# Kernel tuning notes

Hardware: AMD Instinct MI355X
Metric: run time of the kernel (lower is better)

Reference implementation:

```python
import jax, jax.numpy as jnp
import numpy as np

NUM_CODEBOOKS = 8
CODEBOOK_SIZE = 2048
CODEBOOK_DIM = 16
HIDDEN_SIZE = 2048
CODEC_VOCAB_START = 0
PAD_IDX = 0


def setup_inputs() -> dict:
    key = jax.random.key(0)
    k_ids, k_emb, k_w1, k_b1, k_w2, k_b2 = jax.random.split(key, 6)
    B, S = 4, 4096
    codec_input_ids = jax.random.randint(
        k_ids, (B, S), 0, NUM_CODEBOOKS * CODEBOOK_SIZE, dtype=jnp.int64
    )
    # frozen embedding table; padding_idx row is zero
    embed_table = jax.random.normal(
        k_emb, (NUM_CODEBOOKS * CODEBOOK_SIZE, CODEBOOK_DIM), dtype=jnp.float32
    )
    embed_table = embed_table.at[PAD_IDX].set(0.0)
    # per-codebook projector params (stacked over codebook axis k)
    s1 = 1.0 / np.sqrt(CODEBOOK_DIM)
    s2 = 1.0 / np.sqrt(HIDDEN_SIZE)
    W1 = jax.random.uniform(k_w1, (NUM_CODEBOOKS, CODEBOOK_DIM, HIDDEN_SIZE), jnp.float32, -s1, s1)
    b1 = jax.random.uniform(k_b1, (NUM_CODEBOOKS, HIDDEN_SIZE), jnp.float32, -s1, s1)
    W2 = jax.random.uniform(k_w2, (NUM_CODEBOOKS, HIDDEN_SIZE, HIDDEN_SIZE), jnp.float32, -s2, s2)
    b2 = jax.random.uniform(k_b2, (NUM_CODEBOOKS, HIDDEN_SIZE), jnp.float32, -s2, s2)
    return {
        "codec_input_ids": codec_input_ids,
        "embed_table": embed_table,
        "W1": W1,
        "b1": b1,
        "W2": W2,
        "b2": b2,
    }


def reference(codec_input_ids, embed_table, W1, b1, W2, b2):
    ids = codec_input_ids - CODEC_VOCAB_START          # [B, S]
    embeds = embed_table[ids]                          # [B, S, D]
    cb = ids // CODEBOOK_SIZE                          # which codebook each token belongs to
    out = jnp.zeros(ids.shape + (HIDDEN_SIZE,), dtype=embeds.dtype)
    # fixed small loop over structurally distinct per-codebook projectors;
    # disjoint masks cover all tokens, so masked accumulation == torch scatter
    for k in range(NUM_CODEBOOKS):
        h = jnp.einsum("bsd,dh->bsh", embeds, W1[k]) + b1[k]
        h = jax.nn.gelu(h, approximate=False)          # torch nn.GELU default = exact
        h = jnp.einsum("bsh,hg->bsg", h, W2[k]) + b2[k]
        out = out + jnp.where((cb == k)[..., None], h, 0.0)
    return out
```

## Files before the change

### kernel.cpp

```cpp
#include <hip/hip_runtime.h>
#include <hip/hip_bf16.h>
#include <stdint.h>

#define NUM_CB   8
#define CB_BITS  11
#define DIM      16
#define HS       2048
#define NTOK     16384

#define BM 128
#define BN 128
#define BK 32
#define MAXT 160
#define PADCAP (136*BM)

#define OFF_CNT    0u
#define OFF_CUR    32u
#define OFF_NT     64u
#define OFF_GS     96u
#define OFF_TCB    128u
#define OFF_TROW   768u
#define OFF_TVAL   1408u
#define OFF_PERM   2048u
#define OFF_H      71680u
#define OFF_W2T    71374848u
#define WS_NEED    138483712u

typedef __attribute__((ext_vector_type(8))) short s16x8;
typedef __attribute__((ext_vector_type(4))) float f32x4;

__device__ __forceinline__ void load_lds16(const void* g, void* l) {
    __builtin_amdgcn_global_load_lds(
        (const __attribute__((address_space(1))) uint32_t*)g,
        (__attribute__((address_space(3))) uint32_t*)l, 16, 0, 0);
}

extern "C" __global__ void k_countplan(const int* __restrict__ ids,
                                       uint32_t* __restrict__ cur, uint32_t* __restrict__ numT,
                                       uint32_t* __restrict__ tcb, uint32_t* __restrict__ trow,
                                       uint32_t* __restrict__ tval, uint32_t* __restrict__ gstart) {
    __shared__ uint32_t hist[NUM_CB];
    __shared__ uint32_t s_tcb[MAXT], s_trow[MAXT], s_tval[MAXT];
    __shared__ uint32_t s_gs[NUM_CB], s_nt;
    const int tid = threadIdx.x;
    if (tid < NUM_CB) { hist[tid] = 0; cur[tid] = 0; }
    __syncthreads();
    for (int i = tid; i < NTOK; i += 1024)
        atomicAdd(&hist[(uint32_t)ids[i] >> CB_BITS], 1u);
    __syncthreads();
    if (tid == 0) {
        uint32_t ps = 0, nt = 0;
        for (int k = 0; k < NUM_CB; ++k) {
            s_gs[k] = ps;
            uint32_t c = hist[k];
            uint32_t tiles = (c + BM - 1) / BM;
            for (uint32_t m = 0; m < tiles; ++m) {
                s_tcb[nt] = (uint32_t)k;
                s_trow[nt] = ps + m * BM;
                uint32_t rem = c - m * BM;
                s_tval[nt] = rem < BM ? rem : BM;
                ++nt;
            }
            ps += tiles * BM;
        }
        s_nt = nt;
    }
    __syncthreads();
    const uint32_t nt = s_nt;
    if (tid < MAXT) {
        tcb[tid]  = (tid < (int)nt) ? s_tcb[tid] : 0u;
        trow[tid] = (tid < (int)nt) ? s_trow[tid] : 0u;
        tval[tid] = (tid < (int)nt) ? s_tval[tid] : 0u;
    }
    if (tid < NUM_CB) gstart[tid] = s_gs[tid];
    if (tid == 0) *numT = nt;
}

extern "C" __global__ void k_assign(const int* __restrict__ ids, const uint32_t* __restrict__ gstart,
                                    uint32_t* __restrict__ cur, uint32_t* __restrict__ perm) {
    __shared__ uint32_t lh[NUM_CB], lbase[NUM_CB];
    const int tid = threadIdx.x;
    const int t = blockIdx.x * 256 + tid;
    if (tid < NUM_CB) lh[tid] = 0;
    __syncthreads();
    const int cb = (uint32_t)ids[t] >> CB_BITS;
    atomicAdd(&lh[cb], 1u);
    __syncthreads();
    if (tid < NUM_CB) {
        lbase[tid] = lh[tid] ? atomicAdd(&cur[tid], lh[tid]) : 0u;
        lh[tid] = 0;
    }
    __syncthreads();
    const uint32_t r = atomicAdd(&lh[cb], 1u);
    perm[gstart[cb] + lbase[cb] + r] = (uint32_t)t;
}

extern "C" __global__ void k_hbuild(const int* __restrict__ ids, const float* __restrict__ emb,
                                    const float* __restrict__ W1, const float* __restrict__ b1,
                                    const uint32_t* __restrict__ numT, const uint32_t* __restrict__ tcb,
                                    const uint32_t* __restrict__ trow, const uint32_t* __restrict__ tval,
                                    const uint32_t* __restrict__ perm, __hip_bfloat16* __restrict__ H) {
    if (blockIdx.x >= *numT) return;
    const int cb = (int)tcb[blockIdx.x];
    const int row0 = (int)trow[blockIdx.x];
    const int valid = (int)tval[blockIdx.x];
    const int col0 = blockIdx.y * 256;
    const int tid = threadIdx.x;

    __shared__ float es[BM][DIM];
    __shared__ float w1s[DIM][256];
    __shared__ int   rid[BM];

    if (tid < BM) rid[tid] = (tid < valid) ? ids[perm[row0 + tid]] : 0;
    __syncthreads();
    for (int idx = tid; idx < BM * DIM; idx += 256) {
        int r = idx >> 4, d = idx & 15;
        es[r][d] = emb[(size_t)rid[r] * DIM + d];
    }
    const float* W1k = W1 + (size_t)cb * DIM * HS + col0;
    for (int idx = tid; idx < DIM * 256; idx += 256) {
        int d = idx >> 8, c = idx & 255;
        w1s[d][c] = W1k[(size_t)d * HS + c];
    }
    __syncthreads();

    float w[DIM];
    #pragma unroll
    for (int d = 0; d < DIM; ++d) w[d] = w1s[d][tid];
    const float bb = b1[(size_t)cb * HS + col0 + tid];
    __hip_bfloat16* Hc = H + (size_t)row0 * HS + col0 + tid;

    for (int r = 0; r < BM; ++r) {
        const float4 e0 = *(const float4*)&es[r][0];
        const float4 e1 = *(const float4*)&es[r][4];
        const float4 e2 = *(const float4*)&es[r][8];
        const float4 e3 = *(const float4*)&es[r][12];
        float acc = bb;
        acc += e0.x*w[0] + e0.y*w[1] + e0.z*w[2] + e0.w*w[3];
        acc += e1.x*w[4] + e1.y*w[5] + e1.z*w[6] + e1.w*w[7];
        acc += e2.x*w[8] + e2.y*w[9] + e2.z*w[10] + e2.w*w[11];
        acc += e3.x*w[12] + e3.y*w[13] + e3.z*w[14] + e3.w*w[15];
        float g = 0.5f * acc * (1.f + erff(acc * 0.70710678118f));
        Hc[(size_t)r * HS] = __float2bfloat16(g);
    }
}

extern "C" __global__ void k_w2t(const float* __restrict__ W2, __hip_bfloat16* __restrict__ W2T) {
    __shared__ float s[64][65];
    const int k0 = blockIdx.x * 64, n0 = blockIdx.y * 64, cb = blockIdx.z;
    const int tid = threadIdx.x;
    const float* src = W2 + ((size_t)cb << 22);
    #pragma unroll
    for (int i = 0; i < 16; ++i) {
        int idx = i * 256 + tid;
        int kl = idx >> 6, nl = idx & 63;
        s[kl][nl] = src[(size_t)(k0 + kl) * HS + n0 + nl];
    }
    __syncthreads();
    __hip_bfloat16* dst = W2T + ((size_t)cb << 22);
    #pragma unroll
    for (int i = 0; i < 16; ++i) {
        int idx = i * 256 + tid;
        int nl = idx >> 6, kl = idx & 63;
        dst[(size_t)(n0 + nl) * HS + k0 + kl] = __float2bfloat16(s[kl][nl]);
    }
}

extern "C" __global__ void __launch_bounds__(256, 4) k_gemm(
    const __hip_bfloat16* __restrict__ Hb, const __hip_bfloat16* __restrict__ W2Tb,
    const float* __restrict__ b2, const uint32_t* __restrict__ numT,
    const uint32_t* __restrict__ tcb, const uint32_t* __restrict__ trow,
    const uint32_t* __restrict__ tval, const uint32_t* __restrict__ perm,
    float* __restrict__ out)
{
    const int mslot = blockIdx.y;
    if (mslot >= (int)*numT) return;
    const int cb = (int)tcb[mslot];
    const int row0 = (int)trow[mslot];
    const int valid = (int)tval[mslot];
    const int n0 = blockIdx.x * BN;

    const int tid = threadIdx.x;
    const int lane = tid & 63, wave = tid >> 6;
    const int wm = wave >> 1, wn = wave & 1;

    __shared__ __align__(16) unsigned short As[2][4096];
    __shared__ __align__(16) unsigned short Bs[2][4096];

    const unsigned short* H = (const unsigned short*)Hb;
    const unsigned short* W2 = (const unsigned short*)W2Tb;

    const int idx0 = tid, idx1 = 256 + tid;
    const unsigned short* gA0 = H + (size_t)(row0 + (idx0 & 127)) * HS + (idx0 >> 7) * 8;
    const unsigned short* gA1 = H + (size_t)(row0 + (idx1 & 127)) * HS + (idx1 >> 7) * 8;
    const unsigned short* gB0 = W2 + ((size_t)cb * HS + n0 + (idx0 & 127)) * HS + (idx0 >> 7) * 8;
    const unsigned short* gB1 = W2 + ((size_t)cb * HS + n0 + (idx1 & 127)) * HS + (idx1 >> 7) * 8;

    const uint32_t ls0 = (uint32_t)__builtin_amdgcn_readfirstlane(wave * 512);
    const uint32_t ls1 = (uint32_t)__builtin_amdgcn_readfirstlane(2048 + wave * 512);

    f32x4 acc[4][4];
    #pragma unroll
    for (int i = 0; i < 4; ++i)
        #pragma unroll
        for (int j = 0; j < 4; ++j) acc[i][j] = (f32x4){0.f, 0.f, 0.f, 0.f};

    load_lds16(gA0, &As[0][ls0]);
    load_lds16(gA1, &As[0][ls1]);
    load_lds16(gB0, &Bs[0][ls0]);
    load_lds16(gB1, &Bs[0][ls1]);
    __syncthreads();

    const int c = lane >> 4, r = lane & 15;
    uint32_t aoff[4], boff[4];
    #pragma unroll
    for (int f = 0; f < 4; ++f) {
        aoff[f] = c * 1024 + (wm * 64 + f * 16 + r) * 8;
        boff[f] = c * 1024 + (wn * 64 + f * 16 + r) * 8;
    }

    const int NK = HS / BK;
    for (int kk = 0; kk < NK; ++kk) {
        const int curb = kk & 1;
        if (kk + 1 < NK) {
            const int nxt = curb ^ 1;
            const size_t kadv = (size_t)(kk + 1) * BK;
            load_lds16(gA0 + kadv, &As[nxt][ls0]);
            load_lds16(gA1 + kadv, &As[nxt][ls1]);
            load_lds16(gB0 + kadv, &Bs[nxt][ls0]);
            load_lds16(gB1 + kadv, &Bs[nxt][ls1]);
        }
        s16x8 a[4], b[4];
        #pragma unroll
        for (int f = 0; f < 4; ++f) a[f] = *(const s16x8*)&As[curb][aoff[f]];
        #pragma unroll
        for (int f = 0; f < 4; ++f) b[f] = *(const s16x8*)&Bs[curb][boff[f]];
        #pragma unroll
        for (int mf = 0; mf < 4; ++mf)
            #pragma unroll
            for (int nf = 0; nf < 4; ++nf)
                acc[mf][nf] = __builtin_amdgcn_mfma_f32_16x16x32_bf16(a[mf], b[nf], acc[mf][nf], 0, 0, 0);
        __syncthreads();
    }

    const float* b2k = b2 + (size_t)cb * HS;
    const int ncol = n0 + wn * 64 + (lane & 15);
    float bias[4];
    #pragma unroll
    for (int nf = 0; nf < 4; ++nf) bias[nf] = b2k[ncol + nf * 16];

    #pragma unroll
    for (int mf = 0; mf < 4; ++mf) {
        #pragma unroll
        for (int jj = 0; jj < 4; ++jj) {
            const int m = wm * 64 + mf * 16 + (lane >> 4) * 4 + jj;
            if (m < valid) {
                const int orow = (int)perm[row0 + m];
                float* op = out + (size_t)orow * HS;
                #pragma unroll
                for (int nf = 0; nf < 4; ++nf)
                    op[ncol + nf * 16] = acc[mf][nf][jj] + bias[nf];
            }
        }
    }
}

extern "C" void kernel_launch(void* const* d_in, const int* in_sizes, int n_in,
                              void* d_out, int out_size, void* d_ws, size_t ws_size,
                              hipStream_t stream) {
    const int*   ids = (const int*)d_in[0];
    const float* emb = (const float*)d_in[1];
    const float* W1  = (const float*)d_in[2];
    const float* b1  = (const float*)d_in[3];
    const float* W2  = (const float*)d_in[4];
    const float* b2  = (const float*)d_in[5];
    float* out = (float*)d_out;

    if (ws_size < (size_t)WS_NEED) return;

    char* ws = (char*)d_ws;
    uint32_t* cur    = (uint32_t*)(ws + OFF_CUR);
    uint32_t* numT   = (uint32_t*)(ws + OFF_NT);
    uint32_t* gstart = (uint32_t*)(ws + OFF_GS);
    uint32_t* tcb    = (uint32_t*)(ws + OFF_TCB);
    uint32_t* trow   = (uint32_t*)(ws + OFF_TROW);
    uint32_t* tval   = (uint32_t*)(ws + OFF_TVAL);
    uint32_t* perm   = (uint32_t*)(ws + OFF_PERM);
    __hip_bfloat16* Hbf  = (__hip_bfloat16*)(ws + OFF_H);
    __hip_bfloat16* W2Tb = (__hip_bfloat16*)(ws + OFF_W2T);

    k_countplan<<<1, 1024, 0, stream>>>(ids, cur, numT, tcb, trow, tval, gstart);
    k_assign   <<<NTOK / 256, 256, 0, stream>>>(ids, gstart, cur, perm);
    k_w2t      <<<dim3(32, 32, 8), 256, 0, stream>>>(W2, W2Tb);
    k_hbuild   <<<dim3(MAXT, 8), 256, 0, stream>>>(ids, emb, W1, b1, numT, tcb, trow, tval, perm, Hbf);
    k_gemm     <<<dim3(HS / BN, MAXT), 256, 0, stream>>>(Hbf, W2Tb, b2, numT, tcb, trow, tval, perm, out);
}
```

Before: 619.3 us.

## Enlarge GEMM tiles to 256x256 with 8-wave phased pipeline and vectorize helper kernels

The grouped GEMM moves from 128x128x32 tiles with 4 waves to 256x256x64 tiles with 8 waves. It stages k-halves into LDS asynchronously and interleaves MFMA phases with staging, explicit waitcnt, barriers and setprio. Tokens within each codebook are now packed densely, with no tile padding, and rows past the valid count are clamped when loading H. The histogram, embedding/W1 loads and W2 transpose are vectorized, and hbuild skips invalid rows. The aim is more data reuse per LDS load and better latency hiding, at the cost of fewer blocks, since 128 KB of LDS per block limits occupancy.

```diff
diff --git a/kernel.cpp b/kernel.cpp
--- a/kernel.cpp
+++ b/kernel.cpp
@@ -8,31 +8,30 @@
 #define HS       2048
 #define NTOK     16384
 
-#define BM 128
-#define BN 128
-#define BK 32
-#define MAXT 160
-#define PADCAP (136*BM)
-
-#define OFF_CNT    0u
-#define OFF_CUR    32u
+#define BM 256
+#define BN 256
+#define BK 64
+#define NKT (HS / BK)
+#define MAXT 72
+
+#define OFF_CUR    0u
 #define OFF_NT     64u
-#define OFF_GS     96u
-#define OFF_TCB    128u
-#define OFF_TROW   768u
-#define OFF_TVAL   1408u
-#define OFF_PERM   2048u
-#define OFF_H      71680u
-#define OFF_W2T    71374848u
-#define WS_NEED    138483712u
+#define OFF_GS     128u
+#define OFF_TCB    256u
+#define OFF_TROW   1024u
+#define OFF_TVAL   2048u
+#define OFF_PERM   4096u
+#define OFF_H      69632u
+#define OFF_W2T    67178496u
+#define WS_NEED    134287360u
 
 typedef __attribute__((ext_vector_type(8))) short s16x8;
 typedef __attribute__((ext_vector_type(4))) float f32x4;
 
-__device__ __forceinline__ void load_lds16(const void* g, void* l) {
+__device__ __forceinline__ void load_lds16(const void* g, const void* l) {
     __builtin_amdgcn_global_load_lds(
         (const __attribute__((address_space(1))) uint32_t*)g,
-        (__attribute__((address_space(3))) uint32_t*)l, 16, 0, 0);
+        (__attribute__((address_space(3))) uint32_t*)(void*)(uintptr_t)l, 16, 0, 0);
 }
 
 extern "C" __global__ void k_countplan(const int* __restrict__ ids,
@@ -45,8 +44,30 @@
     const int tid = threadIdx.x;
     if (tid < NUM_CB) { hist[tid] = 0; cur[tid] = 0; }
     __syncthreads();
-    for (int i = tid; i < NTOK; i += 1024)
-        atomicAdd(&hist[(uint32_t)ids[i] >> CB_BITS], 1u);
+    uint32_t c0=0,c1=0,c2=0,c3=0,c4=0,c5=0,c6=0,c7=0;
+    const int4* v4 = (const int4*)ids;
+    for (int i = tid; i < NTOK / 4; i += 1024) {
+        int4 v = v4[i];
+        uint32_t a = (uint32_t)v.x >> CB_BITS, b = (uint32_t)v.y >> CB_BITS;
+        uint32_t cc = (uint32_t)v.z >> CB_BITS, d = (uint32_t)v.w >> CB_BITS;
+        c0 += (a==0)+(b==0)+(cc==0)+(d==0);  c1 += (a==1)+(b==1)+(cc==1)+(d==1);
+        c2 += (a==2)+(b==2)+(cc==2)+(d==2);  c3 += (a==3)+(b==3)+(cc==3)+(d==3);
+        c4 += (a==4)+(b==4)+(cc==4)+(d==4);  c5 += (a==5)+(b==5)+(cc==5)+(d==5);
+        c6 += (a==6)+(b==6)+(cc==6)+(d==6);  c7 += (a==7)+(b==7)+(cc==7)+(d==7);
+    }
+    #pragma unroll
+    for (int off = 32; off > 0; off >>= 1) {
+        c0 += __shfl_down(c0, off); c1 += __shfl_down(c1, off);
+        c2 += __shfl_down(c2, off); c3 += __shfl_down(c3, off);
+        c4 += __shfl_down(c4, off); c5 += __shfl_down(c5, off);
+        c6 += __shfl_down(c6, off); c7 += __shfl_down(c7, off);
+    }
+    if ((tid & 63) == 0) {
+        if (c0) atomicAdd(&hist[0], c0); if (c1) atomicAdd(&hist[1], c1);
+        if (c2) atomicAdd(&hist[2], c2); if (c3) atomicAdd(&hist[3], c3);
+        if (c4) atomicAdd(&hist[4], c4); if (c5) atomicAdd(&hist[5], c5);
+        if (c6) atomicAdd(&hist[6], c6); if (c7) atomicAdd(&hist[7], c7);
+    }
     __syncthreads();
     if (tid == 0) {
         uint32_t ps = 0, nt = 0;
@@ -61,7 +82,7 @@
                 s_tval[nt] = rem < BM ? rem : BM;
                 ++nt;
             }
-            ps += tiles * BM;
+            ps += c;
         }
         s_nt = nt;
     }
@@ -111,16 +132,20 @@
     __shared__ float w1s[DIM][256];
     __shared__ int   rid[BM];
 
-    if (tid < BM) rid[tid] = (tid < valid) ? ids[perm[row0 + tid]] : 0;
-    __syncthreads();
-    for (int idx = tid; idx < BM * DIM; idx += 256) {
-        int r = idx >> 4, d = idx & 15;
-        es[r][d] = emb[(size_t)rid[r] * DIM + d];
+    rid[tid] = (tid < valid) ? ids[perm[row0 + tid]] : 0;
+    __syncthreads();
+    #pragma unroll
+    for (int i = 0; i < 4; ++i) {
+        int idx = i * 256 + tid;
+        int r = idx >> 2, q = (idx & 3) * 4;
+        *(float4*)&es[r][q] = *(const float4*)&emb[(size_t)rid[r] * DIM + q];
     }
     const float* W1k = W1 + (size_t)cb * DIM * HS + col0;
-    for (int idx = tid; idx < DIM * 256; idx += 256) {
-        int d = idx >> 8, c = idx & 255;
-        w1s[d][c] = W1k[(size_t)d * HS + c];
+    #pragma unroll
+    for (int i = 0; i < 4; ++i) {
+        int idx = i * 256 + tid;
+        int d = idx >> 6, c4 = (idx & 63) * 4;
+        *(float4*)&w1s[d][c4] = *(const float4*)&W1k[(size_t)d * HS + c4];
     }
     __syncthreads();
 
@@ -131,6 +156,7 @@
     __hip_bfloat16* Hc = H + (size_t)row0 * HS + col0 + tid;
 
     for (int r = 0; r < BM; ++r) {
+        if (r >= valid) break;
         const float4 e0 = *(const float4*)&es[r][0];
         const float4 e1 = *(const float4*)&es[r][4];
         const float4 e2 = *(const float4*)&es[r][8];
@@ -151,22 +177,71 @@
     const int tid = threadIdx.x;
     const float* src = W2 + ((size_t)cb << 22);
     #pragma unroll
-    for (int i = 0; i < 16; ++i) {
+    for (int i = 0; i < 4; ++i) {
         int idx = i * 256 + tid;
-        int kl = idx >> 6, nl = idx & 63;
-        s[kl][nl] = src[(size_t)(k0 + kl) * HS + n0 + nl];
+        int kl = idx >> 4, n4 = (idx & 15) * 4;
+        float4 v = *(const float4*)&src[(size_t)(k0 + kl) * HS + n0 + n4];
+        s[kl][n4] = v.x; s[kl][n4+1] = v.y; s[kl][n4+2] = v.z; s[kl][n4+3] = v.w;
     }
     __syncthreads();
     __hip_bfloat16* dst = W2T + ((size_t)cb << 22);
     #pragma unroll
-    for (int i = 0; i < 16; ++i) {
+    for (int i = 0; i < 4; ++i) {
         int idx = i * 256 + tid;
-        int nl = idx >> 6, kl = idx & 63;
-        dst[(size_t)(n0 + nl) * HS + k0 + kl] = __float2bfloat16(s[kl][nl]);
-    }
-}
-
-extern "C" __global__ void __launch_bounds__(256, 4) k_gemm(
+        int n = idx >> 4, k4 = (idx & 15) * 4;
+        __align__(8) __hip_bfloat16 o[4];
+        o[0] = __float2bfloat16(s[k4+0][n]); o[1] = __float2bfloat16(s[k4+1][n]);
+        o[2] = __float2bfloat16(s[k4+2][n]); o[3] = __float2bfloat16(s[k4+3][n]);
+        *(ushort4*)&dst[(size_t)(n0 + n) * HS + k0 + k4] = *(const ushort4*)o;
+    }
+}
+
+#define MM(m_, a_, n_, b_) acc[m_][n_] = __builtin_amdgcn_mfma_f32_16x16x32_bf16(a_, b_, acc[m_][n_], 0, 0, 0)
+
+#define PHASE(p_, ks_, mh_, STG) do {                                          \
+    const char* Ab_ = sA + (p_)*32768 + (ks_)*16384 + laneA + (mh_)*1024;      \
+    const char* Bb_ = sB + (p_)*32768 + (ks_)*16384 + laneB;                   \
+    s16x8 a0 = *(const s16x8*)(Ab_);                                           \
+    s16x8 a1 = *(const s16x8*)(Ab_ + 256);                                     \
+    s16x8 a2 = *(const s16x8*)(Ab_ + 512);                                     \
+    s16x8 a3 = *(const s16x8*)(Ab_ + 768);                                     \
+    s16x8 bb0 = *(const s16x8*)(Bb_);                                          \
+    s16x8 bb1 = *(const s16x8*)(Bb_ + 256);                                    \
+    s16x8 bb2 = *(const s16x8*)(Bb_ + 512);                                    \
+    s16x8 bb3 = *(const s16x8*)(Bb_ + 768);                                    \
+    STG;                                                                       \
+    __builtin_amdgcn_s_barrier();                                              \
+    asm volatile("s_waitcnt lgkmcnt(0)" ::: "memory");                         \
+    __builtin_amdgcn_sched_barrier(0);                                         \
+    __builtin_amdgcn_s_setprio(1);                                             \
+    MM((mh_)*4+0, a0, 0, bb0); MM((mh_)*4+0, a0, 1, bb1);                      \
+    MM((mh_)*4+0, a0, 2, bb2); MM((mh_)*4+0, a0, 3, bb3);                      \
+    MM((mh_)*4+1, a1, 0, bb0); MM((mh_)*4+1, a1, 1, bb1);                      \
+    MM((mh_)*4+1, a1, 2, bb2); MM((mh_)*4+1, a1, 3, bb3);                      \
+    MM((mh_)*4+2, a2, 0, bb0); MM((mh_)*4+2, a2, 1, bb1);                      \
+    MM((mh_)*4+2, a2, 2, bb2); MM((mh_)*4+2, a2, 3, bb3);                      \
+    MM((mh_)*4+3, a3, 0, bb0); MM((mh_)*4+3, a3, 1, bb1);                      \
+    MM((mh_)*4+3, a3, 2, bb2); MM((mh_)*4+3, a3, 3, bb3);                      \
+    __builtin_amdgcn_s_setprio(0);                                             \
+} while (0)
+
+#define STAGE_A(q_, c47_, koff_) do {                                          \
+    const unsigned short* _g = gA_t + (koff_) + (c47_) * 32;                   \
+    load_lds16(_g,      sA + (q_)*32768 + (c47_)*16384 + wbase);               \
+    load_lds16(_g + 16, sA + (q_)*32768 + (c47_)*16384 + wbase + 8192);        \
+} while (0)
+#define STAGE_B(q_, c47_, koff_) do {                                          \
+    const unsigned short* _g = gB_t + (koff_) + (c47_) * 32;                   \
+    load_lds16(_g,      sB + (q_)*32768 + (c47_)*16384 + wbase);               \
+    load_lds16(_g + 16, sB + (q_)*32768 + (c47_)*16384 + wbase + 8192);        \
+} while (0)
+
+#define VM4 asm volatile("s_waitcnt vmcnt(4)" ::: "memory")
+#define VM0 asm volatile("s_waitcnt vmcnt(0)" ::: "memory")
+#define BAR __builtin_amdgcn_s_barrier()
+#define NOSTG ((void)0)
+
+extern "C" __global__ void __launch_bounds__(512, 2) k_gemm(
     const __hip_bfloat16* __restrict__ Hb, const __hip_bfloat16* __restrict__ W2Tb,
     const float* __restrict__ b2, const uint32_t* __restrict__ numT,
     const uint32_t* __restrict__ tcb, const uint32_t* __restrict__ trow,
@@ -182,84 +257,63 @@
 
     const int tid = threadIdx.x;
     const int lane = tid & 63, wave = tid >> 6;
-    const int wm = wave >> 1, wn = wave & 1;
-
-    __shared__ __align__(16) unsigned short As[2][4096];
-    __shared__ __align__(16) unsigned short Bs[2][4096];
-
-    const unsigned short* H = (const unsigned short*)Hb;
+    const int wm = wave >> 2, wn = wave & 3;
+
+    __shared__ __align__(16) char sA[65536];
+    __shared__ __align__(16) char sB[65536];
+
+    const unsigned short* H  = (const unsigned short*)Hb;
     const unsigned short* W2 = (const unsigned short*)W2Tb;
 
-    const int idx0 = tid, idx1 = 256 + tid;
-    const unsigned short* gA0 = H + (size_t)(row0 + (idx0 & 127)) * HS + (idx0 >> 7) * 8;
-    const unsigned short* gA1 = H + (size_t)(row0 + (idx1 & 127)) * HS + (idx1 >> 7) * 8;
-    const unsigned short* gB0 = W2 + ((size_t)cb * HS + n0 + (idx0 & 127)) * HS + (idx0 >> 7) * 8;
-    const unsigned short* gB1 = W2 + ((size_t)cb * HS + n0 + (idx1 & 127)) * HS + (idx1 >> 7) * 8;
-
-    const uint32_t ls0 = (uint32_t)__builtin_amdgcn_readfirstlane(wave * 512);
-    const uint32_t ls1 = (uint32_t)__builtin_amdgcn_readfirstlane(2048 + wave * 512);
-
-    f32x4 acc[4][4];
-    #pragma unroll
-    for (int i = 0; i < 4; ++i)
+    const int trl = tid & 255;
+    const int rA = trl < valid ? trl : (valid - 1);
+    const unsigned short* gA_t = H  + (size_t)(row0 + rA) * HS + (tid >> 8) * 8;
+    const unsigned short* gB_t = W2 + ((size_t)cb * HS + n0 + trl) * HS + (tid >> 8) * 8;
+    const uint32_t wbase = (uint32_t)__builtin_amdgcn_readfirstlane((uint32_t)(wave << 10));
+
+    const uint32_t laneA = ((uint32_t)(lane >> 4) << 12) + (((uint32_t)(lane & 15) + wm * 128) << 4);
+    const uint32_t laneB = ((uint32_t)(lane >> 4) << 12) + (((uint32_t)(lane & 15) + wn * 64) << 4);
+
+    f32x4 acc[8][4];
+    #pragma unroll
+    for (int i = 0; i < 8; ++i)
         #pragma unroll
         for (int j = 0; j < 4; ++j) acc[i][j] = (f32x4){0.f, 0.f, 0.f, 0.f};
 
-    load_lds16(gA0, &As[0][ls0]);
-    load_lds16(gA1, &As[0][ls1]);
-    load_lds16(gB0, &Bs[0][ls0]);
-    load_lds16(gB1, &Bs[0][ls1]);
-    __syncthreads();
-
-    const int c = lane >> 4, r = lane & 15;
-    uint32_t aoff[4], boff[4];
-    #pragma unroll
-    for (int f = 0; f < 4; ++f) {
-        aoff[f] = c * 1024 + (wm * 64 + f * 16 + r) * 8;
-        boff[f] = c * 1024 + (wn * 64 + f * 16 + r) * 8;
-    }
-
-    const int NK = HS / BK;
-    for (int kk = 0; kk < NK; ++kk) {
-        const int curb = kk & 1;
-        if (kk + 1 < NK) {
-            const int nxt = curb ^ 1;
-            const size_t kadv = (size_t)(kk + 1) * BK;
-            load_lds16(gA0 + kadv, &As[nxt][ls0]);
-            load_lds16(gA1 + kadv, &As[nxt][ls1]);
-            load_lds16(gB0 + kadv, &Bs[nxt][ls0]);
-            load_lds16(gB1 + kadv, &Bs[nxt][ls1]);
-        }
-        s16x8 a[4], b[4];
-        #pragma unroll
-        for (int f = 0; f < 4; ++f) a[f] = *(const s16x8*)&As[curb][aoff[f]];
-        #pragma unroll
-        for (int f = 0; f < 4; ++f) b[f] = *(const s16x8*)&Bs[curb][boff[f]];
-        #pragma unroll
-        for (int mf = 0; mf < 4; ++mf)
-            #pragma unroll
-            for (int nf = 0; nf < 4; ++nf)
-                acc[mf][nf] = __builtin_amdgcn_mfma_f32_16x16x32_bf16(a[mf], b[nf], acc[mf][nf], 0, 0, 0);
-        __syncthreads();
-    }
+    STAGE_A(0, 0, 0); STAGE_B(0, 0, 0); STAGE_A(0, 1, 0); STAGE_B(0, 1, 0);
+    VM4;
+    BAR;
+
+    #pragma unroll 2
+    for (int kt = 0; kt < NKT - 1; ++kt) {
+        const int p = kt & 1, q = p ^ 1;
+        const int koff = (kt + 1) * BK;
+        PHASE(p, 0, 0, STAGE_A(q, 0, koff));      BAR;
+        PHASE(p, 0, 1, STAGE_B(q, 0, koff)); VM4; BAR;
+        PHASE(p, 1, 0, STAGE_A(q, 1, koff));      BAR;
+        PHASE(p, 1, 1, STAGE_B(q, 1, koff)); VM4; BAR;
+    }
+    PHASE(1, 0, 0, NOSTG);      BAR;
+    PHASE(1, 0, 1, NOSTG); VM0; BAR;
+    PHASE(1, 1, 0, NOSTG);      BAR;
+    PHASE(1, 1, 1, NOSTG);
 
     const float* b2k = b2 + (size_t)cb * HS;
-    const int ncol = n0 + wn * 64 + (lane & 15);
+    const int colb = n0 + wn * 64 + (lane & 15);
     float bias[4];
     #pragma unroll
-    for (int nf = 0; nf < 4; ++nf) bias[nf] = b2k[ncol + nf * 16];
-
-    #pragma unroll
-    for (int mf = 0; mf < 4; ++mf) {
+    for (int nf = 0; nf < 4; ++nf) bias[nf] = b2k[colb + nf * 16];
+
+    #pragma unroll
+    for (int mf = 0; mf < 8; ++mf) {
         #pragma unroll
         for (int jj = 0; jj < 4; ++jj) {
-            const int m = wm * 64 + mf * 16 + (lane >> 4) * 4 + jj;
+            const int m = wm * 128 + mf * 16 + (lane >> 4) * 4 + jj;
             if (m < valid) {
-                const int orow = (int)perm[row0 + m];
-                float* op = out + (size_t)orow * HS;
+                float* op = out + (size_t)perm[row0 + m] * HS;
                 #pragma unroll
                 for (int nf = 0; nf < 4; ++nf)
-                    op[ncol + nf * 16] = acc[mf][nf][jj] + bias[nf];
+                    op[colb + nf * 16] = acc[mf][nf][jj] + bias[nf];
             }
         }
     }
@@ -293,5 +347,5 @@
     k_assign   <<<NTOK / 256, 256, 0, stream>>>(ids, gstart, cur, perm);
     k_w2t      <<<dim3(32, 32, 8), 256, 0, stream>>>(W2, W2Tb);
     k_hbuild   <<<dim3(MAXT, 8), 256, 0, stream>>>(ids, emb, W1, b1, numT, tcb, trow, tval, perm, Hbf);
-    k_gemm     <<<dim3(HS / BN, MAXT), 256, 0, stream>>>(Hbf, W2Tb, b2, numT, tcb, trow, tval, perm, out);
-}
+    k_gemm     <<<dim3(HS / BN, MAXT), 512, 0, stream>>>(Hbf, W2Tb, b2, numT, tcb, trow, tval, perm, out);
+}
```

After: 650.5 us. 5.0% more time.
